# Kernel optimization log

Measured on AMD Instinct MI355X. Metric: run time of the kernel, lower is better.

Reference implementation:

```python
import math
import jax, jax.numpy as jnp
import numpy as np

NUM_HEADS = 16
NUM_BUCKETS = 32
MAX_DISTANCE = 128
NEG_INF = -1e9
LN_EPS = 1e-5


def _rel_pos_bias(rab_emb, T):
    # buckets for relative position (i - j) clamped at 0, T5-style log buckets
    i = jnp.arange(T)[:, None]
    j = jnp.arange(T)[None, :]
    n = jnp.clip(i - j, 0, None)  # = -(mem - ctx), clamped min 0
    max_exact = NUM_BUCKETS // 2
    large = max_exact + (
        jnp.log(n.astype(jnp.float32) / max_exact + 1e-6)
        / math.log(MAX_DISTANCE / max_exact)
        * (NUM_BUCKETS - max_exact)
    ).astype(jnp.int32)
    large = jnp.minimum(large, NUM_BUCKETS - 1)
    buckets = jnp.where(n < max_exact, n, large)  # [T, T]
    return rab_emb[buckets].transpose(2, 0, 1)[None]  # [1, H, T, T]


def setup_inputs() -> dict:
    key = jax.random.key(0)
    ks = jax.random.split(key, 8)
    B, T, D = 2, 1024, 1024
    x = jax.random.normal(ks[0], (B, T, D), dtype=jnp.float32)
    # additive causal mask: 0 where allowed, -1e9 where blocked (code tests ==0 for allowed)
    causal_block = jnp.triu(jnp.ones((T, T), dtype=bool), k=1)
    attention_mask = jnp.where(causal_block, NEG_INF, 0.0).astype(jnp.float32)
    # key padding: second sequence has last 256 positions padded
    lengths = jnp.array([T, T - 256])
    key_padding_mask = jnp.arange(T)[None, :] >= lengths[:, None]  # True = pad
    s = 1.0 / math.sqrt(D)
    W_in = jax.random.normal(ks[1], (4 * D, D), dtype=jnp.float32) * s
    b_in = jax.random.normal(ks[2], (4 * D,), dtype=jnp.float32) * 0.02
    W_out = jax.random.normal(ks[3], (D, D), dtype=jnp.float32) * s
    b_out = jax.random.normal(ks[4], (D,), dtype=jnp.float32) * 0.02
    gamma = jnp.ones((D,), dtype=jnp.float32)
    beta = jnp.zeros((D,), dtype=jnp.float32)
    rab_emb = jax.random.normal(ks[5], (NUM_BUCKETS, NUM_HEADS), dtype=jnp.float32) * 0.02
    return {
        "x": x,
        "attention_mask": attention_mask,
        "key_padding_mask": key_padding_mask,
        "W_in": W_in,
        "b_in": b_in,
        "W_out": W_out,
        "b_out": b_out,
        "gamma": gamma,
        "beta": beta,
        "rab_emb": rab_emb,
    }


def reference(x, attention_mask, key_padding_mask, W_in, b_in, W_out, b_out, gamma, beta, rab_emb):
    B, T, D = x.shape
    H = NUM_HEADS
    hd = D // H
    alpha = hd ** (-0.5)

    h = jax.nn.silu(x @ W_in.T + b_in)  # [B, T, 4D]
    U, V, Q, K = jnp.split(h, 4, axis=-1)

    def heads(t):
        return t.reshape(B, T, H, hd).transpose(0, 2, 1, 3)  # [B, H, T, hd]

    Qh, Kh, Vh = heads(Q), heads(K), heads(V)

    rab = _rel_pos_bias(rab_emb, T)  # [1, H, T, T]
    logits = jnp.einsum("bhtd,bhsd->bhts", Qh, Kh) * alpha + rab + attention_mask[None, None]

    valid = (~key_padding_mask).astype(jnp.float32)[:, None, None, :]  # [B,1,1,T]
    allowed = (attention_mask == 0).astype(jnp.float32)[None, None] * valid  # [B,1,T,T] bcast
    # padded keys: torch masked_fill(-inf) then logits_safe -> -1e9
    logits = jnp.where(valid == 0, NEG_INF, logits)

    denom = jnp.clip(jnp.sum(allowed, axis=-1, keepdims=True), 1.0, None)
    attention = jax.nn.silu(logits) / denom  # pointwise SiLU attention, no softmax

    AV = jnp.einsum("bhts,bhsd->bthd", attention, Vh).reshape(B, T, D)

    mu = jnp.mean(AV, axis=-1, keepdims=True)
    var = jnp.var(AV, axis=-1, keepdims=True)
    normed = (AV - mu) / jnp.sqrt(var + LN_EPS) * gamma + beta

    y = (normed * U) @ W_out.T + b_out  # U_flat == U (head reshape round-trips)
    return x + y
```

## Files before the change

kernel.cpp:

```cpp
#include <hip/hip_runtime.h>
#include <stdint.h>

#define DEV static __device__ __forceinline__

typedef unsigned short u16;
typedef float floatx4 __attribute__((ext_vector_type(4)));
typedef short bf16x8 __attribute__((ext_vector_type(8)));
typedef unsigned short ushort8v __attribute__((ext_vector_type(8)));

constexpr int Tn = 1024;
constexpr int Dn = 1024;
constexpr int Hn = 16;
constexpr int FD = 4096;

DEV float b2f(u16 u) { union { unsigned int i; float f; } v; v.i = ((unsigned int)u) << 16; return v.f; }
DEV u16 f2b(float f) {
  union { float f; unsigned int i; } v; v.f = f;
  unsigned int x = v.i;
  x += 0x7fffu + ((x >> 16) & 1u);
  return (u16)(x >> 16);
}

DEV void async16(const void* g, void* l) {
  __builtin_amdgcn_global_load_lds((const __attribute__((address_space(1))) void*)g,
                                   (__attribute__((address_space(3))) void*)l,
                                   16, 0, 0);
}

DEV bool is_bf16(const unsigned* gdet) { return gdet[0] == 0x3F803F80u; }
DEV int kp_mode(const unsigned* kp) {
  unsigned d511 = kp[511];
  if (d511 == 0x01010101u) return 1;
  unsigned d1023 = kp[1023];
  if (d1023 == 0x3F803F80u) return 2;
  unsigned d2047 = kp[2047];
  return (d2047 == 0x3F800000u) ? 3 : 0;
}

__global__ void cvt_big(const void* __restrict__ x, const void* __restrict__ wi,
                        const void* __restrict__ wo, u16* __restrict__ xb,
                        u16* __restrict__ wib, u16* __restrict__ wob,
                        const unsigned* __restrict__ gdet)
{
  if (is_bf16(gdet)) return;
  int i = blockIdx.x * 256 + threadIdx.x;
  const void* src; u16* dst; int j;
  if (i < 524288)       { src = x;  dst = xb;  j = i; }
  else if (i < 1572864) { src = wi; dst = wib; j = i - 524288; }
  else                  { src = wo; dst = wob; j = i - 1572864; }
  float4 v = ((const float4*)src)[j];
  ushort4 o; o.x = f2b(v.x); o.y = f2b(v.y); o.z = f2b(v.z); o.w = f2b(v.w);
  ((ushort4*)dst)[j] = o;
}

__global__ void cvt_small(const void* __restrict__ bi, const void* __restrict__ bo,
                          const void* __restrict__ ga, const void* __restrict__ be,
                          float* __restrict__ smallf)
{
  const bool fbf = is_bf16((const unsigned*)ga);
  int i = blockIdx.x * 256 + threadIdx.x;
  if (i >= 7168) return;
  const void* src; int j;
  if (i < 4096)      { src = bi; j = i; }
  else if (i < 5120) { src = bo; j = i - 4096; }
  else if (i < 6144) { src = ga; j = i - 5120; }
  else               { src = be; j = i - 6144; }
  smallf[i] = fbf ? b2f(((const u16*)src)[j]) : ((const float*)src)[j];
}

__global__ void prep2_kern(const void* __restrict__ kp, const void* __restrict__ rab,
                           const unsigned* __restrict__ gdet,
                           float* __restrict__ biasG, float* __restrict__ denomG,
                           unsigned long long* __restrict__ kmaskG)
{
  const int tid = threadIdx.x;
  if (blockIdx.x == 2) {
    const bool fbf = is_bf16(gdet);
    for (int i = tid; i < Hn * Tn; i += 256) {
      int hh = i >> 10, d = i & 1023;
      int bk;
      if (d < 16) bk = d;
      else {
        float lg = logf((float)d * 0.0625f + 1e-6f) / logf(8.f) * 16.f;
        bk = 16 + (int)lg;
        bk = bk < 31 ? bk : 31;
      }
      int j = bk * Hn + hh;
      biasG[i] = fbf ? b2f(((const u16*)rab)[j]) : ((const float*)rab)[j];
    }
    return;
  }
  const int b = blockIdx.x;
  const int mode = kp_mode((const unsigned*)kp);
  __shared__ unsigned char vb[1024];
  __shared__ int wtot[4];
  int vv[4];
  const int t0 = tid * 4;
#pragma unroll
  for (int i = 0; i < 4; i++) {
    int t = b * Tn + t0 + i;
    int pad;
    if (mode == 0)      pad = (((const int*)kp)[t] != 0);
    else if (mode == 1) pad = (((const unsigned char*)kp)[t] != 0);
    else if (mode == 2) pad = (((const u16*)kp)[t] != 0);
    else                pad = (((const float*)kp)[t] != 0.f);
    vv[i] = pad ? 0 : 1;
    vb[t0 + i] = (unsigned char)vv[i];
  }
  int p1 = vv[0], p2 = p1 + vv[1], p3 = p2 + vv[2], p4 = p3 + vv[3];
  const int lane = tid & 63, w = tid >> 6;
  int ws = p4;
#pragma unroll
  for (int off = 1; off < 64; off <<= 1) {
    int t = __shfl_up(ws, off, 64);
    if (lane >= off) ws += t;
  }
  if (lane == 63) wtot[w] = ws;
  __syncthreads();
  int base = 0;
  for (int j = 0; j < w; j++) base += wtot[j];
  int excl = base + ws - p4;
  int c1 = excl + p1, c2 = excl + p2, c3 = excl + p3, c4 = excl + p4;
  denomG[b * Tn + t0 + 0] = (float)(c1 < 1 ? 1 : c1);
  denomG[b * Tn + t0 + 1] = (float)(c2 < 1 ? 1 : c2);
  denomG[b * Tn + t0 + 2] = (float)(c3 < 1 ? 1 : c3);
  denomG[b * Tn + t0 + 3] = (float)(c4 < 1 ? 1 : c4);
  if (tid < 16) {
    unsigned long long m = 0;
    for (int j = 0; j < 64; j++) m |= (unsigned long long)vb[tid * 64 + j] << j;
    kmaskG[b * 16 + tid] = m;
  }
}

template<int BM, int BN, int WR, int WC, int EPI>
__global__ __launch_bounds__(WR * WC * 64, 2)
void gemm_bt(const u16* __restrict__ Ac, const u16* __restrict__ Ar,
             const u16* __restrict__ Bc, const u16* __restrict__ Br,
             const float* __restrict__ biasf, const void* __restrict__ X,
             void* __restrict__ C, const unsigned* __restrict__ gdet,
             int M, int N, int K)
{
  constexpr int NT = WR * WC * 64;
  __shared__ u16 As[BM * 32];
  __shared__ u16 Bs[BN * 32];
  const int fbf = is_bf16(gdet) ? 1 : 0;
  const u16* A  = fbf ? Ar : Ac;
  const u16* Bm = fbf ? Br : Bc;
  const int tid = threadIdx.x;
  const int lane = tid & 63;
  const int w = tid >> 6;
  const int wm = w / WC, wn = w % WC;
  const int q = lane >> 4, l16 = lane & 15;
  const int rowBase = blockIdx.y * BM;
  const int colBase = blockIdx.x * BN;

  floatx4 acc[4][4];
#pragma unroll
  for (int i = 0; i < 4; i++)
#pragma unroll
    for (int j = 0; j < 4; j++)
#pragma unroll
      for (int r = 0; r < 4; r++) acc[i][j][r] = 0.f;

  for (int kb = 0; kb < K; kb += 32) {
    __syncthreads();
#pragma unroll
    for (int i = 0; i < BM * 4 / NT; i++) {
      int c = i * NT + tid;
      async16(&A[(size_t)(rowBase + (c >> 2)) * K + kb + (c & 3) * 8], &As[c * 8]);
    }
#pragma unroll
    for (int i = 0; i < BN * 4 / NT; i++) {
      int c = i * NT + tid;
      async16(&Bm[(size_t)(colBase + (c >> 2)) * K + kb + (c & 3) * 8], &Bs[c * 8]);
    }
    __syncthreads();
    bf16x8 af[4], bfr[4];
#pragma unroll
    for (int mt = 0; mt < 4; mt++)
      af[mt] = *(const bf16x8*)&As[(wm * 64 + mt * 16 + l16) * 32 + q * 8];
#pragma unroll
    for (int nt = 0; nt < 4; nt++)
      bfr[nt] = *(const bf16x8*)&Bs[(wn * 64 + nt * 16 + l16) * 32 + q * 8];
#pragma unroll
    for (int mt = 0; mt < 4; mt++)
#pragma unroll
      for (int nt = 0; nt < 4; nt++)
        acc[mt][nt] = __builtin_amdgcn_mfma_f32_16x16x32_bf16(af[mt], bfr[nt], acc[mt][nt], 0, 0, 0);
  }

#pragma unroll
  for (int mt = 0; mt < 4; mt++)
#pragma unroll
    for (int nt = 0; nt < 4; nt++) {
      int col = colBase + wn * 64 + nt * 16 + l16;
      float bcol = biasf[col];
#pragma unroll
      for (int r = 0; r < 4; r++) {
        int row = rowBase + wm * 64 + mt * 16 + q * 4 + r;
        size_t idx = (size_t)row * N + col;
        float v = acc[mt][nt][r] + bcol;
        if (EPI == 0) {
          v = v / (1.f + __expf(-v));
          ((u16*)C)[idx] = f2b(v);
        } else {
          float rx = fbf ? b2f(((const u16*)X)[idx]) : ((const float*)X)[idx];
          v += rx;
          if (fbf) ((u16*)C)[idx] = f2b(v);
          else     ((float*)C)[idx] = v;
        }
      }
    }
}

__global__ __launch_bounds__(256)
void vt_kern(const u16* __restrict__ h, u16* __restrict__ VtG)
{
  __shared__ u16 L[4096];
  const int tid = threadIdx.x;
  const int tt = blockIdx.x, head = blockIdx.y, b = blockIdx.z;
  const u16* hb = h + (size_t)b * Tn * FD;
#pragma unroll
  for (int i = 0; i < 2; i++) {
    int s = i * 256 + tid;
    async16(&hb[(size_t)(tt * 64 + (s >> 3)) * FD + 1024 + head * 64 + (s & 7) * 8], &L[s * 8]);
  }
  __syncthreads();
  u16* vout = VtG + ((size_t)(b * Hn + head)) * 64 * Tn;
#pragma unroll
  for (int i = 0; i < 2; i++) {
    int oc = i * 256 + tid;
    int d = oc >> 3, tc = oc & 7;
    ushort8v v;
#pragma unroll
    for (int j = 0; j < 8; j++) v[j] = L[(tc * 8 + j) * 64 + d];
    *(ushort8v*)&vout[(size_t)d * Tn + tt * 64 + tc * 8] = v;
  }
}

__global__ __launch_bounds__(256, 4)
void attn_kern(const u16* __restrict__ h, const u16* __restrict__ VtG,
               const float* __restrict__ biasG, const float* __restrict__ denomG,
               const unsigned long long* __restrict__ kmaskG,
               float* __restrict__ AV)
{
  __shared__ u16 Qs[4096];
  __shared__ u16 Ks[4096];
  __shared__ u16 Vs[4096];
  __shared__ u16 Ps[4096];
  __shared__ float biasL[1024];
  const int tid = threadIdx.x;
  const int lane = tid & 63;
  const int w = tid >> 6;
  const int q = lane >> 4, l16 = lane & 15;

  int qt = 0, rem = blockIdx.x;
  for (;;) { int nc = (qt + 4) >> 2; if (rem < nc) break; rem -= nc; qt++; }
  const int kt0 = rem * 4;
  const int kt1 = (kt0 + 4 < qt + 1) ? kt0 + 4 : qt + 1;
  const bool sole = (kt0 == 0) && (kt1 == qt + 1);

  const int head = blockIdx.y, b = blockIdx.z;
  const u16* hb = h + (size_t)b * Tn * FD;
  const u16* vtb = VtG + ((size_t)(b * Hn + head)) * 64 * Tn;

#pragma unroll
  for (int i = 0; i < 2; i++) {
    int s = i * 256 + tid;
    int row = s >> 3, dc = (s & 7) ^ (row & 7);
    async16(&hb[(size_t)(qt * 64 + row) * FD + 2048 + head * 64 + dc * 8], &Qs[s * 8]);
    async16(&hb[(size_t)(kt0 * 64 + row) * FD + 3072 + head * 64 + dc * 8], &Ks[s * 8]);
    async16(&vtb[(size_t)row * Tn + kt0 * 64 + dc * 8], &Vs[s * 8]);
  }
  async16(&biasG[head * Tn + tid * 4], &biasL[tid * 4]);
  __syncthreads();

  const int sw0 = q ^ (l16 & 7);
  const int qrow = w * 16 + l16;
  bf16x8 bq0 = *(const bf16x8*)&Qs[(qrow * 8 + sw0) * 8];
  bf16x8 bq1 = *(const bf16x8*)&Qs[(qrow * 8 + (sw0 ^ 4)) * 8];
  const float dinv = 1.f / denomG[b * Tn + qt * 64 + qrow];

  floatx4 o[4];
#pragma unroll
  for (int nt = 0; nt < 4; nt++)
#pragma unroll
    for (int r = 0; r < 4; r++) o[nt][r] = 0.f;

  for (int kt = kt0; kt < kt1; kt++) {
    const unsigned long long km = kmaskG[b * 16 + kt];
    const int dq = (qt - kt) * 64 + qrow;
#pragma unroll
    for (int st = 0; st < 4; st++) {
      int rk = (st * 16 + l16) * 8;
      bf16x8 ak0 = *(const bf16x8*)&Ks[(rk + sw0) * 8];
      bf16x8 ak1 = *(const bf16x8*)&Ks[(rk + (sw0 ^ 4)) * 8];
      floatx4 sT;
#pragma unroll
      for (int r = 0; r < 4; r++) sT[r] = 0.f;
      sT = __builtin_amdgcn_mfma_f32_16x16x32_bf16(ak0, bq0, sT, 0, 0, 0);
      sT = __builtin_amdgcn_mfma_f32_16x16x32_bf16(ak1, bq1, sT, 0, 0, 0);
      unsigned mb = (unsigned)(km >> (st * 16 + q * 4)) & 0xFu;
      u16 pr[4];
#pragma unroll
      for (int r = 0; r < 4; r++) {
        int delta = dq - (st * 16 + q * 4 + r);
        float p = 0.f;
        if (((mb >> r) & 1u) && delta >= 0) {
          float xv = sT[r] * 0.125f + biasL[delta];
          p = xv * dinv / (1.f + __expf(-xv));
        }
        pr[r] = f2b(p);
      }
      unsigned lo = pr[0] | ((unsigned)pr[1] << 16);
      unsigned hi = pr[2] | ((unsigned)pr[3] << 16);
      int cch = (st * 2 + (q >> 1)) ^ (l16 & 7);
      *(uint2*)&Ps[w * 1024 + l16 * 64 + cch * 8 + (q & 1) * 4] = make_uint2((unsigned)lo, (unsigned)hi);
    }
    int rp = w * 1024 + l16 * 64;
    bf16x8 ap0 = *(const bf16x8*)&Ps[rp + sw0 * 8];
    bf16x8 ap1 = *(const bf16x8*)&Ps[rp + (sw0 ^ 4) * 8];
#pragma unroll
    for (int nt = 0; nt < 4; nt++) {
      int rv = (nt * 16 + l16) * 8;
      bf16x8 bv0 = *(const bf16x8*)&Vs[(rv + sw0) * 8];
      bf16x8 bv1 = *(const bf16x8*)&Vs[(rv + (sw0 ^ 4)) * 8];
      o[nt] = __builtin_amdgcn_mfma_f32_16x16x32_bf16(ap0, bv0, o[nt], 0, 0, 0);
      o[nt] = __builtin_amdgcn_mfma_f32_16x16x32_bf16(ap1, bv1, o[nt], 0, 0, 0);
    }
    if (kt + 1 < kt1) {
      __syncthreads();
#pragma unroll
      for (int i = 0; i < 2; i++) {
        int s = i * 256 + tid;
        int row = s >> 3, dc = (s & 7) ^ (row & 7);
        async16(&hb[(size_t)((kt + 1) * 64 + row) * FD + 3072 + head * 64 + dc * 8], &Ks[s * 8]);
        async16(&vtb[(size_t)row * Tn + (kt + 1) * 64 + dc * 8], &Vs[s * 8]);
      }
      __syncthreads();
    }
  }

  float* avp = AV + ((size_t)b * Tn + qt * 64 + w * 16 + q * 4) * Dn + head * 64;
#pragma unroll
  for (int nt = 0; nt < 4; nt++)
#pragma unroll
    for (int r = 0; r < 4; r++) {
      float* p = avp + (size_t)r * Dn + nt * 16 + l16;
      if (sole) *p = o[nt][r];
      else __hip_atomic_fetch_add(p, o[nt][r], __ATOMIC_RELAXED, __HIP_MEMORY_SCOPE_AGENT);
    }
}

__global__ __launch_bounds__(256)
void ln_mul(const float* __restrict__ AV, const u16* __restrict__ h,
            const float* __restrict__ gam, const float* __restrict__ bet,
            u16* __restrict__ z)
{
  struct alignas(8) U4 { u16 a, b, c, d; };
  const int row = blockIdx.x;
  const int tid = threadIdx.x;
  const float4 v = ((const float4*)(AV + (size_t)row * Dn))[tid];
  float s  = v.x + v.y + v.z + v.w;
  float s2 = v.x * v.x + v.y * v.y + v.z * v.z + v.w * v.w;
#pragma unroll
  for (int off = 32; off > 0; off >>= 1) {
    s  += __shfl_down(s, off, 64);
    s2 += __shfl_down(s2, off, 64);
  }
  __shared__ float red[8];
  const int lane = tid & 63, w = tid >> 6;
  if (lane == 0) { red[w] = s; red[4 + w] = s2; }
  __syncthreads();
  const float su = red[0] + red[1] + red[2] + red[3];
  const float sq = red[4] + red[5] + red[6] + red[7];
  const float mu = su * (1.f / 1024.f);
  const float var = sq * (1.f / 1024.f) - mu * mu;
  const float rstd = rsqrtf(var + 1e-5f);

  const U4 uu = ((const U4*)(h + (size_t)row * FD))[tid];
  const float4 g4 = ((const float4*)gam)[tid];
  const float4 b4 = ((const float4*)bet)[tid];
  float r0 = ((v.x - mu) * rstd * g4.x + b4.x) * b2f(uu.a);
  float r1 = ((v.y - mu) * rstd * g4.y + b4.y) * b2f(uu.b);
  float r2 = ((v.z - mu) * rstd * g4.z + b4.z) * b2f(uu.c);
  float r3 = ((v.w - mu) * rstd * g4.w + b4.w) * b2f(uu.d);
  U4 outv; outv.a = f2b(r0); outv.b = f2b(r1); outv.c = f2b(r2); outv.d = f2b(r3);
  ((U4*)(z + (size_t)row * Dn))[tid] = outv;
}

extern "C" void kernel_launch(void* const* d_in, const int* in_sizes, int n_in,
                              void* d_out, int out_size, void* d_ws, size_t ws_size,
                              hipStream_t stream)
{
  const void* x     = d_in[0];
  const void* kp    = d_in[2];
  const void* W_in  = d_in[3];
  const void* b_in  = d_in[4];
  const void* W_out = d_in[5];
  const void* b_out = d_in[6];
  const void* gamma = d_in[7];
  const void* beta  = d_in[8];
  const void* rab   = d_in[9];
  const unsigned* gdet = (const unsigned*)gamma;

  char* ws = (char*)d_ws;
  u16*   h     = (u16*)(ws);
  float* AV    = (float*)(ws + 16777216);
  u16*   z     = (u16*)(ws + 25165824);
  u16*   xb    = (u16*)(ws + 29360128);
  u16*   Wib   = (u16*)(ws + 33554432);
  u16*   VtG   = (u16*)(ws + 33554432);
  u16*   Wob   = (u16*)(ws + 41943040);
  float* smallf= (float*)(ws + 44040192);
  float* biasG = (float*)(ws + 44070912);
  float* denom = (float*)(ws + 44136448);
  unsigned long long* kmask = (unsigned long long*)(ws + 44144640);

  cvt_big<<<7168, 256, 0, stream>>>(x, W_in, W_out, xb, Wib, Wob, gdet);
  cvt_small<<<28, 256, 0, stream>>>(b_in, b_out, gamma, beta, smallf);
  prep2_kern<<<3, 256, 0, stream>>>(kp, rab, gdet, biasG, denom, kmask);
  gemm_bt<128, 128, 2, 2, 0><<<dim3(32, 16), dim3(256), 0, stream>>>(
      xb, (const u16*)x, Wib, (const u16*)W_in, smallf, (const void*)nullptr,
      h, gdet, 2048, 4096, 1024);
  vt_kern<<<dim3(16, 16, 2), dim3(256), 0, stream>>>(h, VtG);
  hipMemsetAsync(AV, 0, 8388608, stream);
  attn_kern<<<dim3(40, 16, 2), dim3(256), 0, stream>>>(h, VtG, biasG, denom, kmask, AV);
  ln_mul<<<2048, 256, 0, stream>>>(AV, h, smallf + 5120, smallf + 6144, z);
  gemm_bt<64, 128, 1, 2, 1><<<dim3(8, 32), dim3(128), 0, stream>>>(
      z, z, Wob, (const u16*)W_out, smallf + 4096, x, d_out, gdet, 2048, 1024, 1024);
}
```

Measured before the change: 213.2 us.

## Replace attention atomics with partial buffers and split-K the output GEMM

Attention key ranges are now split into 1 to 3 chunks depending on the query tile. Each chunk writes its own partial AV buffer, which removes the memset and the atomic adds, and ln_mul sums the partials. The output projection now uses 128x128 tiles with a 4-way split-K into fp32 partials, and a new reduce kernel adds the partials, the bias and the residual. cvt_big also processes four elements per thread. The cost is extra global traffic for the partial buffers, one additional launch and a larger workspace.

```diff
diff --git a/kernel.cpp b/kernel.cpp
--- a/kernel.cpp
+++ b/kernel.cpp
@@ -36,6 +36,7 @@
   unsigned d2047 = kp[2047];
   return (d2047 == 0x3F800000u) ? 3 : 0;
 }
+DEV int nchunks(int qt) { return (qt < 6) ? 1 : ((qt < 12) ? 2 : 3); }
 
 __global__ void cvt_big(const void* __restrict__ x, const void* __restrict__ wi,
                         const void* __restrict__ wo, u16* __restrict__ xb,
@@ -43,14 +44,18 @@
                         const unsigned* __restrict__ gdet)
 {
   if (is_bf16(gdet)) return;
-  int i = blockIdx.x * 256 + threadIdx.x;
-  const void* src; u16* dst; int j;
-  if (i < 524288)       { src = x;  dst = xb;  j = i; }
-  else if (i < 1572864) { src = wi; dst = wib; j = i - 524288; }
-  else                  { src = wo; dst = wob; j = i - 1572864; }
-  float4 v = ((const float4*)src)[j];
-  ushort4 o; o.x = f2b(v.x); o.y = f2b(v.y); o.z = f2b(v.z); o.w = f2b(v.w);
-  ((ushort4*)dst)[j] = o;
+  int i0 = blockIdx.x * 256 + threadIdx.x;
+#pragma unroll
+  for (int k = 0; k < 4; k++) {
+    int i = i0 + k * 458752;
+    const void* src; u16* dst; int j;
+    if (i < 524288)       { src = x;  dst = xb;  j = i; }
+    else if (i < 1572864) { src = wi; dst = wib; j = i - 524288; }
+    else                  { src = wo; dst = wob; j = i - 1572864; }
+    float4 v = ((const float4*)src)[j];
+    ushort4 o; o.x = f2b(v.x); o.y = f2b(v.y); o.z = f2b(v.z); o.w = f2b(v.w);
+    ((ushort4*)dst)[j] = o;
+  }
 }
 
 __global__ void cvt_small(const void* __restrict__ bi, const void* __restrict__ bo,
@@ -136,9 +141,8 @@
 __global__ __launch_bounds__(WR * WC * 64, 2)
 void gemm_bt(const u16* __restrict__ Ac, const u16* __restrict__ Ar,
              const u16* __restrict__ Bc, const u16* __restrict__ Br,
-             const float* __restrict__ biasf, const void* __restrict__ X,
-             void* __restrict__ C, const unsigned* __restrict__ gdet,
-             int M, int N, int K)
+             const float* __restrict__ biasf, void* __restrict__ C,
+             const unsigned* __restrict__ gdet, int M, int N, int K)
 {
   constexpr int NT = WR * WC * 64;
   __shared__ u16 As[BM * 32];
@@ -153,6 +157,8 @@
   const int q = lane >> 4, l16 = lane & 15;
   const int rowBase = blockIdx.y * BM;
   const int colBase = blockIdx.x * BN;
+  const int ksl = K / gridDim.z;
+  const int kb0 = blockIdx.z * ksl;
 
   floatx4 acc[4][4];
 #pragma unroll
@@ -162,7 +168,7 @@
 #pragma unroll
       for (int r = 0; r < 4; r++) acc[i][j][r] = 0.f;
 
-  for (int kb = 0; kb < K; kb += 32) {
+  for (int kb = kb0; kb < kb0 + ksl; kb += 32) {
     __syncthreads();
 #pragma unroll
     for (int i = 0; i < BM * 4 / NT; i++) {
@@ -189,12 +195,13 @@
         acc[mt][nt] = __builtin_amdgcn_mfma_f32_16x16x32_bf16(af[mt], bfr[nt], acc[mt][nt], 0, 0, 0);
   }
 
+  const size_t pOff = (size_t)blockIdx.z * M * N;
 #pragma unroll
   for (int mt = 0; mt < 4; mt++)
 #pragma unroll
     for (int nt = 0; nt < 4; nt++) {
       int col = colBase + wn * 64 + nt * 16 + l16;
-      float bcol = biasf[col];
+      float bcol = (EPI == 0) ? biasf[col] : 0.f;
 #pragma unroll
       for (int r = 0; r < 4; r++) {
         int row = rowBase + wm * 64 + mt * 16 + q * 4 + r;
@@ -204,13 +211,39 @@
           v = v / (1.f + __expf(-v));
           ((u16*)C)[idx] = f2b(v);
         } else {
-          float rx = fbf ? b2f(((const u16*)X)[idx]) : ((const float*)X)[idx];
-          v += rx;
-          if (fbf) ((u16*)C)[idx] = f2b(v);
-          else     ((float*)C)[idx] = v;
+          ((float*)C)[pOff + idx] = v;
         }
       }
     }
+}
+
+__global__ __launch_bounds__(256)
+void reduce2(const float* __restrict__ Gp, const void* __restrict__ X,
+             const float* __restrict__ bout, void* __restrict__ out,
+             const unsigned* __restrict__ gdet)
+{
+  const int fbf = is_bf16(gdet) ? 1 : 0;
+  const int row = blockIdx.x;
+  const int tid = threadIdx.x;
+  const size_t ridx = (size_t)row * Dn;
+  float4 a = ((const float4*)(Gp + ridx))[tid];
+#pragma unroll
+  for (int ks = 1; ks < 4; ks++) {
+    float4 p = ((const float4*)(Gp + (size_t)ks * 2097152 + ridx))[tid];
+    a.x += p.x; a.y += p.y; a.z += p.z; a.w += p.w;
+  }
+  float4 bb = ((const float4*)bout)[tid];
+  a.x += bb.x; a.y += bb.y; a.z += bb.z; a.w += bb.w;
+  if (fbf) {
+    ushort4 xv = ((const ushort4*)X)[ridx / 4 + tid];
+    a.x += b2f(xv.x); a.y += b2f(xv.y); a.z += b2f(xv.z); a.w += b2f(xv.w);
+    ushort4 o; o.x = f2b(a.x); o.y = f2b(a.y); o.z = f2b(a.z); o.w = f2b(a.w);
+    ((ushort4*)out)[ridx / 4 + tid] = o;
+  } else {
+    float4 xv = ((const float4*)X)[ridx / 4 + tid];
+    a.x += xv.x; a.y += xv.y; a.z += xv.z; a.w += xv.w;
+    ((float4*)out)[ridx / 4 + tid] = a;
+  }
 }
 
 __global__ __launch_bounds__(256)
@@ -255,10 +288,12 @@
   const int q = lane >> 4, l16 = lane & 15;
 
   int qt = 0, rem = blockIdx.x;
-  for (;;) { int nc = (qt + 4) >> 2; if (rem < nc) break; rem -= nc; qt++; }
-  const int kt0 = rem * 4;
-  const int kt1 = (kt0 + 4 < qt + 1) ? kt0 + 4 : qt + 1;
-  const bool sole = (kt0 == 0) && (kt1 == qt + 1);
+  for (;;) { int P = nchunks(qt); if (rem < P) break; rem -= P; qt++; }
+  const int c = rem;
+  const int P = nchunks(qt);
+  const int n = qt + 1, cb = n / P, cr = n % P;
+  const int kt0 = c * cb + (c < cr ? c : cr);
+  const int kt1 = kt0 + cb + (c < cr ? 1 : 0);
 
   const int head = blockIdx.y, b = blockIdx.z;
   const u16* hb = h + (size_t)b * Tn * FD;
@@ -315,7 +350,7 @@
       unsigned lo = pr[0] | ((unsigned)pr[1] << 16);
       unsigned hi = pr[2] | ((unsigned)pr[3] << 16);
       int cch = (st * 2 + (q >> 1)) ^ (l16 & 7);
-      *(uint2*)&Ps[w * 1024 + l16 * 64 + cch * 8 + (q & 1) * 4] = make_uint2((unsigned)lo, (unsigned)hi);
+      *(uint2*)&Ps[w * 1024 + l16 * 64 + cch * 8 + (q & 1) * 4] = make_uint2(lo, hi);
     }
     int rp = w * 1024 + l16 * 64;
     bf16x8 ap0 = *(const bf16x8*)&Ps[rp + sw0 * 8];
@@ -341,15 +376,13 @@
     }
   }
 
-  float* avp = AV + ((size_t)b * Tn + qt * 64 + w * 16 + q * 4) * Dn + head * 64;
+  float* avp = AV + (size_t)c * 2097152
+             + ((size_t)b * Tn + qt * 64 + w * 16 + q * 4) * Dn + head * 64;
 #pragma unroll
   for (int nt = 0; nt < 4; nt++)
 #pragma unroll
-    for (int r = 0; r < 4; r++) {
-      float* p = avp + (size_t)r * Dn + nt * 16 + l16;
-      if (sole) *p = o[nt][r];
-      else __hip_atomic_fetch_add(p, o[nt][r], __ATOMIC_RELAXED, __HIP_MEMORY_SCOPE_AGENT);
-    }
+    for (int r = 0; r < 4; r++)
+      avp[(size_t)r * Dn + nt * 16 + l16] = o[nt][r];
 }
 
 __global__ __launch_bounds__(256)
@@ -360,7 +393,16 @@
   struct alignas(8) U4 { u16 a, b, c, d; };
   const int row = blockIdx.x;
   const int tid = threadIdx.x;
-  const float4 v = ((const float4*)(AV + (size_t)row * Dn))[tid];
+  const int P = nchunks(row >> 6 & 15);
+  float4 v = ((const float4*)(AV + (size_t)row * Dn))[tid];
+  if (P > 1) {
+    float4 p = ((const float4*)(AV + 2097152 + (size_t)row * Dn))[tid];
+    v.x += p.x; v.y += p.y; v.z += p.z; v.w += p.w;
+  }
+  if (P > 2) {
+    float4 p = ((const float4*)(AV + 4194304 + (size_t)row * Dn))[tid];
+    v.x += p.x; v.y += p.y; v.z += p.z; v.w += p.w;
+  }
   float s  = v.x + v.y + v.z + v.w;
   float s2 = v.x * v.x + v.y * v.y + v.z * v.z + v.w * v.w;
 #pragma unroll
@@ -407,26 +449,26 @@
   char* ws = (char*)d_ws;
   u16*   h     = (u16*)(ws);
   float* AV    = (float*)(ws + 16777216);
-  u16*   z     = (u16*)(ws + 25165824);
-  u16*   xb    = (u16*)(ws + 29360128);
-  u16*   Wib   = (u16*)(ws + 33554432);
-  u16*   VtG   = (u16*)(ws + 33554432);
-  u16*   Wob   = (u16*)(ws + 41943040);
-  float* smallf= (float*)(ws + 44040192);
-  float* biasG = (float*)(ws + 44070912);
-  float* denom = (float*)(ws + 44136448);
-  unsigned long long* kmask = (unsigned long long*)(ws + 44144640);
-
-  cvt_big<<<7168, 256, 0, stream>>>(x, W_in, W_out, xb, Wib, Wob, gdet);
+  u16*   z     = (u16*)(ws + 41943040);
+  u16*   xb    = (u16*)(ws + 46137344);
+  u16*   Wib   = (u16*)(ws + 50331648);
+  u16*   VtG   = (u16*)(ws + 50331648);
+  u16*   Wob   = (u16*)(ws + 58720256);
+  float* Gp    = (float*)(ws + 60817408);
+  float* smallf= (float*)(ws + 94371840);
+  float* biasG = (float*)(ws + 94400512);
+  float* denom = (float*)(ws + 94466048);
+  unsigned long long* kmask = (unsigned long long*)(ws + 94474240);
+
+  cvt_big<<<1792, 256, 0, stream>>>(x, W_in, W_out, xb, Wib, Wob, gdet);
   cvt_small<<<28, 256, 0, stream>>>(b_in, b_out, gamma, beta, smallf);
   prep2_kern<<<3, 256, 0, stream>>>(kp, rab, gdet, biasG, denom, kmask);
-  gemm_bt<128, 128, 2, 2, 0><<<dim3(32, 16), dim3(256), 0, stream>>>(
-      xb, (const u16*)x, Wib, (const u16*)W_in, smallf, (const void*)nullptr,
-      h, gdet, 2048, 4096, 1024);
+  gemm_bt<128, 128, 2, 2, 0><<<dim3(32, 16, 1), dim3(256), 0, stream>>>(
+      xb, (const u16*)x, Wib, (const u16*)W_in, smallf, h, gdet, 2048, 4096, 1024);
   vt_kern<<<dim3(16, 16, 2), dim3(256), 0, stream>>>(h, VtG);
-  hipMemsetAsync(AV, 0, 8388608, stream);
-  attn_kern<<<dim3(40, 16, 2), dim3(256), 0, stream>>>(h, VtG, biasG, denom, kmask, AV);
+  attn_kern<<<dim3(30, 16, 2), dim3(256), 0, stream>>>(h, VtG, biasG, denom, kmask, AV);
   ln_mul<<<2048, 256, 0, stream>>>(AV, h, smallf + 5120, smallf + 6144, z);
-  gemm_bt<64, 128, 1, 2, 1><<<dim3(8, 32), dim3(128), 0, stream>>>(
-      z, z, Wob, (const u16*)W_out, smallf + 4096, x, d_out, gdet, 2048, 1024, 1024);
-}
+  gemm_bt<128, 128, 2, 2, 2><<<dim3(8, 16, 4), dim3(256), 0, stream>>>(
+      z, z, Wob, (const u16*)W_out, smallf, Gp, gdet, 2048, 1024, 1024);
+  reduce2<<<2048, 256, 0, stream>>>(Gp, x, smallf + 4096, d_out, gdet);
+}
```

Measured after the change: 194.8 us. 1.09x faster.
